# Performance work log

Measured on AMD Instinct MI355X. Metric: run time of the kernel, lower is better.

The kernel has to match this reference:

```python
import jax, jax.numpy as jnp
import numpy as np


def setup_inputs() -> dict:
    key = jax.random.key(0)
    k1, k2 = jax.random.split(key)
    x = jax.random.normal(k1, (32, 128, 64, 64), dtype=jnp.float32)
    weight = jax.random.normal(k2, (256, 128, 3, 3), dtype=jnp.float32)
    return {"x": x, "weight": weight}


def reference(x, weight):
    # Batched VALID cross-correlation, stride 1 (same math as the triple loop
    # of single-channel conv2d calls summed over in_channels).
    # x: [B, Cin, H, W]; weight: [Cout, Cin, k, k] -> out: [B, Cout, H-k+1, W-k+1]
    return jax.lax.conv_general_dilated(
        x, weight,
        window_strides=(1, 1),
        padding="VALID",
        dimension_numbers=("NCHW", "OIHW", "NCHW"),
    )
```

## Files before the change

kernel.cpp:

```cpp
#include <hip/hip_runtime.h>


using bf16x8 = __attribute__((ext_vector_type(8))) __bf16;
using f32x4  = __attribute__((ext_vector_type(4))) float;
using f32x16 = __attribute__((ext_vector_type(16))) float;

constexpr int CIN  = 128;
constexpr int HW   = 64;
constexpr int COUT = 256;
constexpr int OW   = 62;
constexpr int NS   = 62 * 62;
constexpr int NTOT = 32 * NS;
constexpr int KTOT = 9 * CIN;
constexpr int BM = 128, BN = 128, BK = 64;
constexpr int NT = KTOT / BK;
constexpr int NWG = 2 * (NTOT / BN);

constexpr size_t AP_BYTES = (size_t)COUT * KTOT * 2;
constexpr size_t XP_BYTES = (size_t)32 * HW * HW * CIN * 2;
constexpr size_t WS_NEEDED = AP_BYTES + XP_BYTES;

constexpr int BUF  = 32768;
constexpr int BOFF = 16384;

__device__ __forceinline__ unsigned short f2bf(float f) {
  unsigned u = __float_as_uint(f);
  u += 0x7fffu + ((u >> 16) & 1u);
  return (unsigned short)(u >> 16);
}
__device__ __forceinline__ unsigned pack2(float a, float b) {
  return (unsigned)f2bf(a) | ((unsigned)f2bf(b) << 16);
}

__device__ __forceinline__ void gld16(const void* g, void* l) {
  __builtin_amdgcn_global_load_lds(
      (const __attribute__((address_space(1))) unsigned int*)g,
      (__attribute__((address_space(3))) unsigned int*)l, 16, 0, 0);
}


__global__ __launch_bounds__(256)
void prepack_w(const float* __restrict__ w, unsigned* __restrict__ ap32) {
  const int idx = blockIdx.x * 256 + threadIdx.x;
  const int co  = idx / 576;
  const int k2  = idx - co * 576;
  const int k   = k2 * 2;
  const int tap = k >> 7;
  const int ci  = k & 127;
  const float v0 = w[(co * 128 + ci) * 9 + tap];
  const float v1 = w[(co * 128 + ci + 1) * 9 + tap];
  ap32[idx] = pack2(v0, v1);
}

__global__ __launch_bounds__(256)
void prepack_x(const float* __restrict__ x, unsigned* __restrict__ xp32) {
  const int bh = blockIdx.x;
  const int b  = bh >> 6, h = bh & 63;
  const int t  = threadIdx.x;
  const int c  = t & 63;
  const int w0 = (t >> 6) * 16;

  const float* p0 = x + (((size_t)(b * 128 + 2 * c) * HW) + h) * HW + w0;
  const float* p1 = p0 + (size_t)HW * HW;
  float r0[16], r1[16];
#pragma unroll
  for (int j = 0; j < 4; ++j) {
    *reinterpret_cast<float4*>(&r0[j * 4]) = reinterpret_cast<const float4*>(p0)[j];
    *reinterpret_cast<float4*>(&r1[j * 4]) = reinterpret_cast<const float4*>(p1)[j];
  }
  unsigned* o = xp32 + ((size_t)bh * HW + w0) * 64 + c;
#pragma unroll
  for (int j = 0; j < 16; ++j)
    o[j * 64] = pack2(r0[j], r1[j]);
}


__global__ __launch_bounds__(256, 2)
void conv_main(const unsigned short* __restrict__ Ap,
               const unsigned short* __restrict__ Xp,
               float* __restrict__ out) {
  __shared__ __align__(16) char lds[2 * BUF];

  const int tid  = threadIdx.x;
  const int lane = tid & 63;
  const int wid  = tid >> 6;
  const int wm   = wid >> 1;
  const int wn   = wid & 1;

  int wg;
  {
    const int f = blockIdx.x;
    constexpr int q = NWG / 8, r = NWG % 8;
    const int xc = f % 8, p = f / 8;
    wg = (xc < r ? xc * (q + 1) : r * (q + 1) + (xc - r) * q) + p;
  }
  const int co_base = (wg & 1) * BM;
  const int n_base  = (wg >> 1) * BN;

  const int l3  = lane >> 3;
  const int sw8 = ((lane & 7) ^ l3) * 8;
  int aoff[4];
  unsigned xoff[4];
#pragma unroll
  for (int q = 0; q < 4; ++q) {
    const int rr = wid * 32 + q * 8 + l3;
    aoff[q] = (co_base + rr) * KTOT + sw8;
    const unsigned n  = n_base + rr;
    const unsigned bi = n / NS;
    const unsigned s0 = n - bi * NS;
    const unsigned oh = s0 / OW;
    const unsigned ww = s0 - oh * OW;
    xoff[q] = ((bi * HW + oh) * HW + ww) * CIN + sw8;
  }

  const int cl = lane & 31;
  const int gl = lane >> 5;
  int sA[4];
#pragma unroll
  for (int kf = 0; kf < 4; ++kf)
    sA[kf] = ((kf * 2 + gl) ^ (lane & 7)) * 16;
  const int abase = (wm * 64 + cl) * 128;
  const int bbase = BOFF + (wn * 64 + cl) * 128;

  f32x16 acc[2][2] = {};

  auto STAGE = [&](int t, char* dst) {
    const int tap = t >> 1;
    const int kh  = tap / 3;
    const int kw  = tap - kh * 3;
    const int ak  = tap * CIN + (t & 1) * 64;
    const int xk  = (kh * HW + kw) * CIN + (t & 1) * 64;
#pragma unroll
    for (int q = 0; q < 4; ++q)
      gld16(Ap + aoff[q] + ak, dst + (wid * 32 + q * 8) * 128);
#pragma unroll
    for (int q = 0; q < 4; ++q)
      gld16(Xp + xoff[q] + xk, dst + BOFF + (wid * 32 + q * 8) * 128);
  };

  STAGE(0, lds);

#pragma unroll
  for (int t = 0; t < NT; ++t) {
    const char* cur = lds + (t & 1) * BUF;
    asm volatile("s_waitcnt vmcnt(0)" ::: "memory");
    __builtin_amdgcn_s_barrier();
    if (t + 1 < NT) STAGE(t + 1, lds + ((t + 1) & 1) * BUF);

    bf16x8 a[2][4], b[2][4];
#pragma unroll
    for (int mt = 0; mt < 2; ++mt)
#pragma unroll
      for (int kf = 0; kf < 4; ++kf)
        a[mt][kf] = *reinterpret_cast<const bf16x8*>(cur + abase + mt * 4096 + sA[kf]);
#pragma unroll
    for (int nt = 0; nt < 2; ++nt)
#pragma unroll
      for (int kf = 0; kf < 4; ++kf)
        b[nt][kf] = *reinterpret_cast<const bf16x8*>(cur + bbase + nt * 4096 + sA[kf]);

#pragma unroll
    for (int kf = 0; kf < 4; ++kf)
#pragma unroll
      for (int mt = 0; mt < 2; ++mt)
#pragma unroll
        for (int nt = 0; nt < 2; ++nt)
          acc[mt][nt] = __builtin_amdgcn_mfma_f32_32x32x16_bf16(
              a[mt][kf], b[nt][kf], acc[mt][nt], 0, 0, 0);
  }

#pragma unroll
  for (int mt = 0; mt < 2; ++mt)
#pragma unroll
    for (int nt = 0; nt < 2; ++nt) {
      const unsigned n  = n_base + wn * 64 + nt * 32 + cl;
      const unsigned b2 = n / NS;
      const unsigned s2 = n - b2 * NS;
      float* op = out + (size_t)b2 * (COUT * NS) + s2
                      + (size_t)(co_base + wm * 64 + mt * 32 + gl * 4) * NS;
#pragma unroll
      for (int r = 0; r < 16; ++r)
        op[((r & 3) + 8 * (r >> 2)) * NS] = acc[mt][nt][r];
    }
}


__global__ __launch_bounds__(256)
void conv_fallback(const float* __restrict__ x, const float* __restrict__ w,
                   float* __restrict__ out) {
  __shared__ __align__(16) unsigned short As[128 * 32];
  __shared__ __align__(16) unsigned short Bs[128 * 32];

  const int t    = threadIdx.x;
  const int lane = t & 63;
  const int wid  = t >> 6;
  const int wm   = wid >> 1;
  const int wn   = wid & 1;
  const int co_base = blockIdx.x * 128;
  const int n_base  = blockIdx.y * 128;

  const int bn  = t & 127;
  const int bg0 = t >> 7;
  const unsigned n0   = n_base + bn;
  const unsigned bidx = n0 / NS;
  const unsigned s0   = n0 - bidx * NS;
  const unsigned oh   = s0 / OW;
  const unsigned ow   = s0 - oh * OW;
  const float* xb = x + (bidx * (CIN * HW * HW) + oh * HW + ow);

  const int am  = t & 127;
  const int ag0 = (t >> 7) * 2;
  const float* wb = w + (co_base + am) * KTOT;

  f32x4 acc[4][4] = {};

  for (int ks = 0; ks < 36; ++ks) {
    const int tap = ks >> 2;
    const int ci0 = (ks & 3) * 32;
    const int kh  = tap / 3;
    const int kw  = tap - kh * 3;
    const int xo  = kh * HW + kw;

    float av[2][8], bv[2][8];
#pragma unroll
    for (int gi = 0; gi < 2; ++gi) {
      const int g = ag0 + gi;
#pragma unroll
      for (int j = 0; j < 8; ++j)
        av[gi][j] = wb[(ci0 + g * 8 + j) * 9 + tap];
    }
#pragma unroll
    for (int gi = 0; gi < 2; ++gi) {
      const int g = bg0 + gi * 2;
#pragma unroll
      for (int j = 0; j < 8; ++j)
        bv[gi][j] = xb[xo + (ci0 + g * 8 + j) * (HW * HW)];
    }

    __syncthreads();

#pragma unroll
    for (int gi = 0; gi < 2; ++gi) {
      const int g = ag0 + gi;
      uint4 pv;
      pv.x = pack2(av[gi][0], av[gi][1]);
      pv.y = pack2(av[gi][2], av[gi][3]);
      pv.z = pack2(av[gi][4], av[gi][5]);
      pv.w = pack2(av[gi][6], av[gi][7]);
      *reinterpret_cast<uint4*>(&As[am * 32 + ((g ^ ((am >> 1) & 3)) << 3)]) = pv;
    }
#pragma unroll
    for (int gi = 0; gi < 2; ++gi) {
      const int g = bg0 + gi * 2;
      uint4 pv;
      pv.x = pack2(bv[gi][0], bv[gi][1]);
      pv.y = pack2(bv[gi][2], bv[gi][3]);
      pv.z = pack2(bv[gi][4], bv[gi][5]);
      pv.w = pack2(bv[gi][6], bv[gi][7]);
      *reinterpret_cast<uint4*>(&Bs[bn * 32 + ((g ^ ((bn >> 1) & 3)) << 3)]) = pv;
    }

    __syncthreads();

    bf16x8 af[4], bfr[4];
    const int g = lane >> 4;
#pragma unroll
    for (int mi = 0; mi < 4; ++mi) {
      const int m = wm * 64 + mi * 16 + (lane & 15);
      af[mi] = *reinterpret_cast<const bf16x8*>(&As[m * 32 + ((g ^ ((m >> 1) & 3)) << 3)]);
    }
#pragma unroll
    for (int ni = 0; ni < 4; ++ni) {
      const int nn = wn * 64 + ni * 16 + (lane & 15);
      bfr[ni] = *reinterpret_cast<const bf16x8*>(&Bs[nn * 32 + ((g ^ ((nn >> 1) & 3)) << 3)]);
    }
#pragma unroll
    for (int mi = 0; mi < 4; ++mi)
#pragma unroll
      for (int ni = 0; ni < 4; ++ni)
        acc[mi][ni] = __builtin_amdgcn_mfma_f32_16x16x32_bf16(af[mi], bfr[ni],
                                                              acc[mi][ni], 0, 0, 0);
  }

#pragma unroll
  for (int ni = 0; ni < 4; ++ni) {
    const unsigned n  = n_base + wn * 64 + ni * 16 + (lane & 15);
    const unsigned b2 = n / NS;
    const unsigned s2 = n - b2 * NS;
    float* op = out + (size_t)b2 * (COUT * NS) + s2
                    + (size_t)(co_base + wm * 64 + (lane >> 4) * 4) * NS;
#pragma unroll
    for (int mi = 0; mi < 4; ++mi)
#pragma unroll
      for (int r = 0; r < 4; ++r)
        op[(mi * 16 + r) * NS] = acc[mi][ni][r];
  }
}

extern "C" void kernel_launch(void* const* d_in, const int* in_sizes, int n_in,
                              void* d_out, int out_size, void* d_ws, size_t ws_size,
                              hipStream_t stream) {
  const float* x = (const float*)d_in[0];
  const float* w = (const float*)d_in[1];
  float* out = (float*)d_out;

  if (ws_size >= WS_NEEDED) {
    unsigned* ap32 = (unsigned*)d_ws;
    unsigned short* Ap = (unsigned short*)d_ws;
    unsigned short* Xp = (unsigned short*)((char*)d_ws + AP_BYTES);
    unsigned* xp32 = (unsigned*)Xp;
    prepack_w<<<576, 256, 0, stream>>>(w, ap32);
    prepack_x<<<32 * HW, 256, 0, stream>>>(x, xp32);
    conv_main<<<dim3(NWG), 256, 0, stream>>>(Ap, Xp, out);
  } else {
    conv_fallback<<<dim3(2, NTOT / 128), 256, 0, stream>>>(x, w, out);
  }
}
```

Baseline: 110.2 us.

## Widen tile to all output channels and triple-buffer a shallower K step

Each workgroup now covers all 256 output channels for 128 output pixels, so each staged input tile is reused twice as often. This also halves the number of workgroups and the repeated input-patch loads. The K step shrinks from 64 to 32 and the single double buffer becomes a three-stage LDS ring with a partial vmcnt wait, so two stages of prefetch stay in flight. MFMA issue is bracketed with s_setprio, and the LDS swizzle is reworked for the new 64-byte rows. The cost is 128 accumulator registers per thread, more LDS, and more barriers per K.

```diff
diff --git a/kernel.cpp b/kernel.cpp
--- a/kernel.cpp
+++ b/kernel.cpp
@@ -12,15 +12,15 @@
 constexpr int NS   = 62 * 62;
 constexpr int NTOT = 32 * NS;
 constexpr int KTOT = 9 * CIN;
-constexpr int BM = 128, BN = 128, BK = 64;
-constexpr int NT = KTOT / BK;
-constexpr int NWG = 2 * (NTOT / BN);
+constexpr int BN = 128, BK = 32;
+constexpr int NSTEP = KTOT / BK;
+constexpr int NWG = NTOT / BN;
 
 constexpr size_t AP_BYTES = (size_t)COUT * KTOT * 2;
 constexpr size_t XP_BYTES = (size_t)32 * HW * HW * CIN * 2;
 constexpr size_t WS_NEEDED = AP_BYTES + XP_BYTES;
 
-constexpr int BUF  = 32768;
+constexpr int SBUF = 24576;
 constexpr int BOFF = 16384;
 
 __device__ __forceinline__ unsigned short f2bf(float f) {
@@ -79,7 +79,7 @@
 void conv_main(const unsigned short* __restrict__ Ap,
                const unsigned short* __restrict__ Xp,
                float* __restrict__ out) {
-  __shared__ __align__(16) char lds[2 * BUF];
+  __shared__ __align__(16) char lds[3 * SBUF];
 
   const int tid  = threadIdx.x;
   const int lane = tid & 63;
@@ -91,93 +91,98 @@
   {
     const int f = blockIdx.x;
     constexpr int q = NWG / 8, r = NWG % 8;
-    const int xc = f % 8, p = f / 8;
+    const int xc = f & 7, p = f >> 3;
     wg = (xc < r ? xc * (q + 1) : r * (q + 1) + (xc - r) * q) + p;
   }
-  const int co_base = (wg & 1) * BM;
-  const int n_base  = (wg >> 1) * BN;
-
-  const int l3  = lane >> 3;
-  const int sw8 = ((lane & 7) ^ l3) * 8;
+  const int n_base = wg * BN;
+
+  const int lrow2 = ((lane >> 3) << 1) + ((lane >> 2) & 1);
+  const int g8    = ((lane & 3) ^ ((lane >> 3) & 3)) * 8;
   int aoff[4];
-  unsigned xoff[4];
 #pragma unroll
   for (int q = 0; q < 4; ++q) {
-    const int rr = wid * 32 + q * 8 + l3;
-    aoff[q] = (co_base + rr) * KTOT + sw8;
-    const unsigned n  = n_base + rr;
+    const int row = (wid * 4 + q) * 16 + lrow2;
+    aoff[q] = row * KTOT + g8;
+  }
+  unsigned xoff[2];
+#pragma unroll
+  for (int q = 0; q < 2; ++q) {
+    const int rn = (wid * 2 + q) * 16 + lrow2;
+    const unsigned n  = n_base + rn;
     const unsigned bi = n / NS;
     const unsigned s0 = n - bi * NS;
     const unsigned oh = s0 / OW;
     const unsigned ww = s0 - oh * OW;
-    xoff[q] = ((bi * HW + oh) * HW + ww) * CIN + sw8;
+    xoff[q] = ((bi * HW + oh) * HW + ww) * CIN + g8;
   }
 
   const int cl = lane & 31;
   const int gl = lane >> 5;
-  int sA[4];
-#pragma unroll
-  for (int kf = 0; kf < 4; ++kf)
-    sA[kf] = ((kf * 2 + gl) ^ (lane & 7)) * 16;
-  const int abase = (wm * 64 + cl) * 128;
-  const int bbase = BOFF + (wn * 64 + cl) * 128;
-
-  f32x16 acc[2][2] = {};
+  const int q4 = (cl >> 1) & 3;
+  const int sw0 = ((gl)     ^ q4) * 16;
+  const int sw1 = ((2 + gl) ^ q4) * 16;
+  const int ABASE = ((wm * 64 + (cl >> 1)) * 128) + (cl & 1) * 64;
+  const int BBASE = BOFF + ((wn * 32 + (cl >> 1)) * 128) + (cl & 1) * 64;
+
+  f32x16 acc[4][2] = {};
 
   auto STAGE = [&](int t, char* dst) {
-    const int tap = t >> 1;
+    const int tap = t >> 2;
     const int kh  = tap / 3;
     const int kw  = tap - kh * 3;
-    const int ak  = tap * CIN + (t & 1) * 64;
-    const int xk  = (kh * HW + kw) * CIN + (t & 1) * 64;
+    const int ak  = t * BK;
+    const int xk  = (kh * HW + kw) * CIN + (t & 3) * BK;
 #pragma unroll
     for (int q = 0; q < 4; ++q)
-      gld16(Ap + aoff[q] + ak, dst + (wid * 32 + q * 8) * 128);
-#pragma unroll
-    for (int q = 0; q < 4; ++q)
-      gld16(Xp + xoff[q] + xk, dst + BOFF + (wid * 32 + q * 8) * 128);
+      gld16(Ap + aoff[q] + ak, dst + (wid * 4 + q) * 1024);
+#pragma unroll
+    for (int q = 0; q < 2; ++q)
+      gld16(Xp + xoff[q] + xk, dst + BOFF + (wid * 2 + q) * 1024);
   };
 
   STAGE(0, lds);
-
-#pragma unroll
-  for (int t = 0; t < NT; ++t) {
-    const char* cur = lds + (t & 1) * BUF;
-    asm volatile("s_waitcnt vmcnt(0)" ::: "memory");
+  STAGE(1, lds + SBUF);
+
+#pragma unroll
+  for (int t = 0; t < NSTEP; ++t) {
+    const char* cur = lds + (t % 3) * SBUF;
+    if (t < NSTEP - 1) asm volatile("s_waitcnt vmcnt(6)" ::: "memory");
+    else               asm volatile("s_waitcnt vmcnt(0)" ::: "memory");
     __builtin_amdgcn_s_barrier();
-    if (t + 1 < NT) STAGE(t + 1, lds + ((t + 1) & 1) * BUF);
-
-    bf16x8 a[2][4], b[2][4];
-#pragma unroll
-    for (int mt = 0; mt < 2; ++mt)
-#pragma unroll
-      for (int kf = 0; kf < 4; ++kf)
-        a[mt][kf] = *reinterpret_cast<const bf16x8*>(cur + abase + mt * 4096 + sA[kf]);
-#pragma unroll
-    for (int nt = 0; nt < 2; ++nt)
-#pragma unroll
-      for (int kf = 0; kf < 4; ++kf)
-        b[nt][kf] = *reinterpret_cast<const bf16x8*>(cur + bbase + nt * 4096 + sA[kf]);
-
-#pragma unroll
-    for (int kf = 0; kf < 4; ++kf)
-#pragma unroll
-      for (int mt = 0; mt < 2; ++mt)
+    __builtin_amdgcn_sched_barrier(0);
+    if (t + 2 < NSTEP) STAGE(t + 2, lds + ((t + 2) % 3) * SBUF);
+
+#pragma unroll
+    for (int kf = 0; kf < 2; ++kf) {
+      const int sw = kf ? sw1 : sw0;
+      bf16x8 a[4], b[2];
+#pragma unroll
+      for (int mt = 0; mt < 4; ++mt)
+        a[mt] = *reinterpret_cast<const bf16x8*>(cur + ABASE + mt * 2048 + sw);
+#pragma unroll
+      for (int nt = 0; nt < 2; ++nt)
+        b[nt] = *reinterpret_cast<const bf16x8*>(cur + BBASE + nt * 2048 + sw);
+
+      __builtin_amdgcn_s_setprio(1);
+#pragma unroll
+      for (int mt = 0; mt < 4; ++mt)
 #pragma unroll
         for (int nt = 0; nt < 2; ++nt)
           acc[mt][nt] = __builtin_amdgcn_mfma_f32_32x32x16_bf16(
-              a[mt][kf], b[nt][kf], acc[mt][nt], 0, 0, 0);
-  }
-
-#pragma unroll
-  for (int mt = 0; mt < 2; ++mt)
+              a[mt], b[nt], acc[mt][nt], 0, 0, 0);
+      __builtin_amdgcn_s_setprio(0);
+    }
+  }
+
+#pragma unroll
+  for (int mt = 0; mt < 4; ++mt)
 #pragma unroll
     for (int nt = 0; nt < 2; ++nt) {
       const unsigned n  = n_base + wn * 64 + nt * 32 + cl;
       const unsigned b2 = n / NS;
       const unsigned s2 = n - b2 * NS;
       float* op = out + (size_t)b2 * (COUT * NS) + s2
-                      + (size_t)(co_base + wm * 64 + mt * 32 + gl * 4) * NS;
+                      + (size_t)(wm * 128 + mt * 32 + gl * 4) * NS;
 #pragma unroll
       for (int r = 0; r < 16; ++r)
         op[((r & 3) + 8 * (r >> 2)) * NS] = acc[mt][nt][r];
```

Measured after the change: 110.9 us. About the same (+0.6%).

## Halve K-tile to 32 with new LDS swizzle to fit four workgroups per CU

Applied to the files above, without the earlier changes.

Reduces the K step from 64 to 32, halving the double-buffered LDS footprint to 32KB. The launch bound rises to four workgroups per SM/CU to raise occupancy. The LDS row layout and XOR swizzle are reworked so each 16-byte load covers half of a 64-byte row pair. This doubles the number of barriers and stages per tile, and the tighter register budget may cause spills.

```diff
diff --git a/kernel.cpp b/kernel.cpp
--- a/kernel.cpp
+++ b/kernel.cpp
@@ -12,16 +12,16 @@
 constexpr int NS   = 62 * 62;
 constexpr int NTOT = 32 * NS;
 constexpr int KTOT = 9 * CIN;
-constexpr int BM = 128, BN = 128, BK = 64;
-constexpr int NT = KTOT / BK;
+constexpr int BM = 128, BN = 128, BK = 32;
+constexpr int NSTEP = KTOT / BK;
 constexpr int NWG = 2 * (NTOT / BN);
 
 constexpr size_t AP_BYTES = (size_t)COUT * KTOT * 2;
 constexpr size_t XP_BYTES = (size_t)32 * HW * HW * CIN * 2;
 constexpr size_t WS_NEEDED = AP_BYTES + XP_BYTES;
 
-constexpr int BUF  = 32768;
-constexpr int BOFF = 16384;
+constexpr int BUF    = 16384;
+constexpr int BOFF_B = 8192;
 
 __device__ __forceinline__ unsigned short f2bf(float f) {
   unsigned u = __float_as_uint(f);
@@ -75,7 +75,7 @@
 }
 
 
-__global__ __launch_bounds__(256, 2)
+__global__ __launch_bounds__(256, 4)
 void conv_main(const unsigned short* __restrict__ Ap,
                const unsigned short* __restrict__ Xp,
                float* __restrict__ out) {
@@ -97,70 +97,70 @@
   const int co_base = (wg & 1) * BM;
   const int n_base  = (wg >> 1) * BN;
 
-  const int l3  = lane >> 3;
-  const int sw8 = ((lane & 7) ^ l3) * 8;
-  int aoff[4];
-  unsigned xoff[4];
-#pragma unroll
-  for (int q = 0; q < 4; ++q) {
-    const int rr = wid * 32 + q * 8 + l3;
-    aoff[q] = (co_base + rr) * KTOT + sw8;
+  const int lrow2 = ((lane >> 3) << 1) + ((lane >> 2) & 1);
+  const int g8    = ((lane & 3) ^ ((lane >> 3) & 3)) * 8;
+  int aoff[2];
+  unsigned xoff[2];
+#pragma unroll
+  for (int q = 0; q < 2; ++q) {
+    const int rr = (wid * 2 + q) * 16 + lrow2;
+    aoff[q] = (co_base + rr) * KTOT + g8;
     const unsigned n  = n_base + rr;
     const unsigned bi = n / NS;
     const unsigned s0 = n - bi * NS;
     const unsigned oh = s0 / OW;
     const unsigned ww = s0 - oh * OW;
-    xoff[q] = ((bi * HW + oh) * HW + ww) * CIN + sw8;
+    xoff[q] = ((bi * HW + oh) * HW + ww) * CIN + g8;
   }
 
   const int cl = lane & 31;
   const int gl = lane >> 5;
-  int sA[4];
-#pragma unroll
-  for (int kf = 0; kf < 4; ++kf)
-    sA[kf] = ((kf * 2 + gl) ^ (lane & 7)) * 16;
-  const int abase = (wm * 64 + cl) * 128;
-  const int bbase = BOFF + (wn * 64 + cl) * 128;
+  const int q4 = (cl >> 1) & 3;
+  int swz[4];
+#pragma unroll
+  for (int kf = 0; kf < 2; ++kf)
+    swz[kf] = (((kf * 2 + gl)) ^ q4) * 16;
+  const int abase0 = (wm * 32 + (cl >> 1)) * 128 + (cl & 1) * 64;
+  const int bbase0 = BOFF_B + (wn * 32 + (cl >> 1)) * 128 + (cl & 1) * 64;
 
   f32x16 acc[2][2] = {};
 
   auto STAGE = [&](int t, char* dst) {
-    const int tap = t >> 1;
+    const int tap = t >> 2;
     const int kh  = tap / 3;
     const int kw  = tap - kh * 3;
-    const int ak  = tap * CIN + (t & 1) * 64;
-    const int xk  = (kh * HW + kw) * CIN + (t & 1) * 64;
-#pragma unroll
-    for (int q = 0; q < 4; ++q)
-      gld16(Ap + aoff[q] + ak, dst + (wid * 32 + q * 8) * 128);
-#pragma unroll
-    for (int q = 0; q < 4; ++q)
-      gld16(Xp + xoff[q] + xk, dst + BOFF + (wid * 32 + q * 8) * 128);
+    const int xk  = (kh * HW + kw) * CIN + (t & 3) * 32;
+#pragma unroll
+    for (int q = 0; q < 2; ++q)
+      gld16(Ap + aoff[q] + t * 32, dst + (wid * 2 + q) * 1024);
+#pragma unroll
+    for (int q = 0; q < 2; ++q)
+      gld16(Xp + xoff[q] + xk, dst + BOFF_B + (wid * 2 + q) * 1024);
   };
 
   STAGE(0, lds);
 
 #pragma unroll
-  for (int t = 0; t < NT; ++t) {
+  for (int t = 0; t < NSTEP; ++t) {
     const char* cur = lds + (t & 1) * BUF;
     asm volatile("s_waitcnt vmcnt(0)" ::: "memory");
     __builtin_amdgcn_s_barrier();
-    if (t + 1 < NT) STAGE(t + 1, lds + ((t + 1) & 1) * BUF);
-
-    bf16x8 a[2][4], b[2][4];
+    if (t + 1 < NSTEP) STAGE(t + 1, lds + ((t + 1) & 1) * BUF);
+
+    bf16x8 a[2][2], b[2][2];
 #pragma unroll
     for (int mt = 0; mt < 2; ++mt)
 #pragma unroll
-      for (int kf = 0; kf < 4; ++kf)
-        a[mt][kf] = *reinterpret_cast<const bf16x8*>(cur + abase + mt * 4096 + sA[kf]);
+      for (int kf = 0; kf < 2; ++kf)
+        a[mt][kf] = *reinterpret_cast<const bf16x8*>(cur + abase0 + mt * 2048 + swz[kf]);
 #pragma unroll
     for (int nt = 0; nt < 2; ++nt)
 #pragma unroll
-      for (int kf = 0; kf < 4; ++kf)
-        b[nt][kf] = *reinterpret_cast<const bf16x8*>(cur + bbase + nt * 4096 + sA[kf]);
-
-#pragma unroll
-    for (int kf = 0; kf < 4; ++kf)
+      for (int kf = 0; kf < 2; ++kf)
+        b[nt][kf] = *reinterpret_cast<const bf16x8*>(cur + bbase0 + nt * 2048 + swz[kf]);
+
+#pragma unroll
+    for (int kf = 0; kf < 2; ++kf)
 #pragma unroll
       for (int mt = 0; mt < 2; ++mt)
 #pragma unroll
```

Result: slower. 121.4 us (+10.2%).

## Load B operand directly from global into registers, double-buffered, bypassing LDS

Applied to the files above, without the earlier changes.

The activation (B) tile is no longer staged through LDS. Each lane now loads its MFMA B fragments straight from the prepacked NHWC bf16 buffer into a register double buffer, one K-step ahead. Only the weight tile still goes through LDS, which halves LDS usage and cuts LDS reads and writes. The wait changes from vmcnt(0) to vmcnt(8) so the next step's loads stay in flight. The costs are more VGPR pressure, direct global loads per lane that are less coalesced and duplicated across the two wm waves, and a dependence on vmcnt ordering for correctness.

```diff
diff --git a/kernel.cpp b/kernel.cpp
--- a/kernel.cpp
+++ b/kernel.cpp
@@ -12,16 +12,15 @@
 constexpr int NS   = 62 * 62;
 constexpr int NTOT = 32 * NS;
 constexpr int KTOT = 9 * CIN;
-constexpr int BM = 128, BN = 128, BK = 64;
-constexpr int NT = KTOT / BK;
+constexpr int BM = 128, BN = 128;
+constexpr int NT = 18;
 constexpr int NWG = 2 * (NTOT / BN);
 
 constexpr size_t AP_BYTES = (size_t)COUT * KTOT * 2;
 constexpr size_t XP_BYTES = (size_t)32 * HW * HW * CIN * 2;
 constexpr size_t WS_NEEDED = AP_BYTES + XP_BYTES;
 
-constexpr int BUF  = 32768;
-constexpr int BOFF = 16384;
+constexpr int ABUF = 16384;
 
 __device__ __forceinline__ unsigned short f2bf(float f) {
   unsigned u = __float_as_uint(f);
@@ -31,7 +30,6 @@
 __device__ __forceinline__ unsigned pack2(float a, float b) {
   return (unsigned)f2bf(a) | ((unsigned)f2bf(b) << 16);
 }
-
 __device__ __forceinline__ void gld16(const void* g, void* l) {
   __builtin_amdgcn_global_load_lds(
       (const __attribute__((address_space(1))) unsigned int*)g,
@@ -47,9 +45,7 @@
   const int k   = k2 * 2;
   const int tap = k >> 7;
   const int ci  = k & 127;
-  const float v0 = w[(co * 128 + ci) * 9 + tap];
-  const float v1 = w[(co * 128 + ci + 1) * 9 + tap];
-  ap32[idx] = pack2(v0, v1);
+  ap32[idx] = pack2(w[(co * 128 + ci) * 9 + tap], w[(co * 128 + ci + 1) * 9 + tap]);
 }
 
 __global__ __launch_bounds__(256)
@@ -59,7 +55,6 @@
   const int t  = threadIdx.x;
   const int c  = t & 63;
   const int w0 = (t >> 6) * 16;
-
   const float* p0 = x + (((size_t)(b * 128 + 2 * c) * HW) + h) * HW + w0;
   const float* p1 = p0 + (size_t)HW * HW;
   float r0[16], r1[16];
@@ -79,7 +74,7 @@
 void conv_main(const unsigned short* __restrict__ Ap,
                const unsigned short* __restrict__ Xp,
                float* __restrict__ out) {
-  __shared__ __align__(16) char lds[2 * BUF];
+  __shared__ __align__(16) char lds[2 * ABUF];
 
   const int tid  = threadIdx.x;
   const int lane = tid & 63;
@@ -100,64 +95,76 @@
   const int l3  = lane >> 3;
   const int sw8 = ((lane & 7) ^ l3) * 8;
   int aoff[4];
-  unsigned xoff[4];
 #pragma unroll
   for (int q = 0; q < 4; ++q) {
     const int rr = wid * 32 + q * 8 + l3;
     aoff[q] = (co_base + rr) * KTOT + sw8;
-    const unsigned n  = n_base + rr;
+  }
+
+  const int cl = lane & 31;
+  const int gl = lane >> 5;
+  int sA[4];
+#pragma unroll
+  for (int kf = 0; kf < 4; ++kf)
+    sA[kf] = ((kf * 2 + gl) ^ (lane & 7)) * 16;
+  const int abase = (wm * 64 + cl) * 128;
+
+  unsigned xbase[2];
+#pragma unroll
+  for (int nt = 0; nt < 2; ++nt) {
+    const unsigned n  = n_base + wn * 64 + nt * 32 + cl;
     const unsigned bi = n / NS;
     const unsigned s0 = n - bi * NS;
     const unsigned oh = s0 / OW;
     const unsigned ww = s0 - oh * OW;
-    xoff[q] = ((bi * HW + oh) * HW + ww) * CIN + sw8;
-  }
-
-  const int cl = lane & 31;
-  const int gl = lane >> 5;
-  int sA[4];
-#pragma unroll
-  for (int kf = 0; kf < 4; ++kf)
-    sA[kf] = ((kf * 2 + gl) ^ (lane & 7)) * 16;
-  const int abase = (wm * 64 + cl) * 128;
-  const int bbase = BOFF + (wn * 64 + cl) * 128;
+    xbase[nt] = ((bi * HW + oh) * HW + ww) * CIN + gl * 8;
+  }
 
   f32x16 acc[2][2] = {};
 
-  auto STAGE = [&](int t, char* dst) {
+  auto STAGE_A = [&](int t, char* dst) {
+    const int tap = t >> 1;
+    const int ak  = tap * CIN + (t & 1) * 64;
+#pragma unroll
+    for (int q = 0; q < 4; ++q)
+      gld16(Ap + aoff[q] + ak, dst + (wid * 32 + q * 8) * 128);
+  };
+  auto LOAD_B = [&](int t, bf16x8 (*b)[4]) {
     const int tap = t >> 1;
     const int kh  = tap / 3;
     const int kw  = tap - kh * 3;
-    const int ak  = tap * CIN + (t & 1) * 64;
-    const int xk  = (kh * HW + kw) * CIN + (t & 1) * 64;
-#pragma unroll
-    for (int q = 0; q < 4; ++q)
-      gld16(Ap + aoff[q] + ak, dst + (wid * 32 + q * 8) * 128);
-#pragma unroll
-    for (int q = 0; q < 4; ++q)
-      gld16(Xp + xoff[q] + xk, dst + BOFF + (wid * 32 + q * 8) * 128);
+    const int ko  = (kh * HW + kw) * CIN + (t & 1) * 64;
+#pragma unroll
+    for (int nt = 0; nt < 2; ++nt)
+#pragma unroll
+      for (int kf = 0; kf < 4; ++kf)
+        b[nt][kf] = *reinterpret_cast<const bf16x8*>(Xp + xbase[nt] + ko + kf * 16);
   };
 
-  STAGE(0, lds);
+  bf16x8 b0[2][4], b1[2][4];
+  STAGE_A(0, lds);
+  LOAD_B(0, b0);
 
 #pragma unroll
   for (int t = 0; t < NT; ++t) {
-    const char* cur = lds + (t & 1) * BUF;
-    asm volatile("s_waitcnt vmcnt(0)" ::: "memory");
+    const char* cur = lds + (t & 1) * ABUF;
+    asm volatile("s_waitcnt vmcnt(8)" ::: "memory");
     __builtin_amdgcn_s_barrier();
-    if (t + 1 < NT) STAGE(t + 1, lds + ((t + 1) & 1) * BUF);
-
-    bf16x8 a[2][4], b[2][4];
+    __builtin_amdgcn_sched_barrier(0);
+
+    if (t + 1 < NT) {
+      STAGE_A(t + 1, lds + ((t + 1) & 1) * ABUF);
+      LOAD_B(t + 1, (t & 1) ? b0 : b1);
+    }
+
+    bf16x8 a[2][4];
 #pragma unroll
     for (int mt = 0; mt < 2; ++mt)
 #pragma unroll
       for (int kf = 0; kf < 4; ++kf)
         a[mt][kf] = *reinterpret_cast<const bf16x8*>(cur + abase + mt * 4096 + sA[kf]);
-#pragma unroll
-    for (int nt = 0; nt < 2; ++nt)
-#pragma unroll
-      for (int kf = 0; kf < 4; ++kf)
-        b[nt][kf] = *reinterpret_cast<const bf16x8*>(cur + bbase + nt * 4096 + sA[kf]);
+
+    const bf16x8 (*bc)[4] = (t & 1) ? b1 : b0;
 
 #pragma unroll
     for (int kf = 0; kf < 4; ++kf)
@@ -166,7 +173,7 @@
 #pragma unroll
         for (int nt = 0; nt < 2; ++nt)
           acc[mt][nt] = __builtin_amdgcn_mfma_f32_32x32x16_bf16(
-              a[mt][kf], b[nt][kf], acc[mt][nt], 0, 0, 0);
+              a[mt][kf], bc[nt][kf], acc[mt][nt], 0, 0, 0);
   }
 
 #pragma unroll
```

Result: slower. 185.2 us (+68.0%).
